# Performance work log

Measured on AMD Instinct MI355X. Metric: run time of the kernel, lower is better.

The kernel has to match this reference:

```python
import jax, jax.numpy as jnp
import numpy as np

L = 4        # routed layers
E = 12       # experts
NH = 4       # attention heads
C = 256      # hidden_dim
M = 128      # mlp_dim
TOPK = 1
LN_EPS = 1e-5


def setup_inputs() -> dict:
    key = jax.random.key(0)
    ks = jax.random.split(key, 16)
    B, H, W = 128, 14, 14

    def w(k, shape, s=0.02):
        return jax.random.normal(k, shape, dtype=jnp.float32) * s

    return {
        'stem_out': jax.random.normal(ks[0], (B, C, H, W), dtype=jnp.float32),
        'gate_w': w(ks[1], (L, C, E)), 'gate_b': jnp.zeros((L, E), jnp.float32),
        'ln1_g': jnp.ones((L, E, C), jnp.float32), 'ln1_b': jnp.zeros((L, E, C), jnp.float32),
        'wq': w(ks[2], (L, E, C, C)), 'bq': jnp.zeros((L, E, C), jnp.float32),
        'wk': w(ks[3], (L, E, C, C)), 'bk': jnp.zeros((L, E, C), jnp.float32),
        'wv': w(ks[4], (L, E, C, C)), 'bv': jnp.zeros((L, E, C), jnp.float32),
        'wo': w(ks[5], (L, E, C, C)), 'bo': jnp.zeros((L, E, C), jnp.float32),
        'ln2_g': jnp.ones((L, E, C), jnp.float32), 'ln2_b': jnp.zeros((L, E, C), jnp.float32),
        'w1': w(ks[6], (L, E, C, M)), 'b1': jnp.zeros((L, E, M), jnp.float32),
        'w2': w(ks[7], (L, E, M, C)), 'b2': jnp.zeros((L, E, C), jnp.float32),
    }


def _ln(x, g, b):
    mu = x.mean(axis=-1, keepdims=True)
    var = ((x - mu) ** 2).mean(axis=-1, keepdims=True)
    return (x - mu) * jax.lax.rsqrt(var + LN_EPS) * g + b


def _vit_block(x, p):
    # x: (B, H, W, C); p: per-expert params (no expert axis)
    B, H, W, Cc = x.shape
    d = Cc // NH
    h = _ln(x, p['g1'], p['bb1'])
    q = h @ p['wq'] + p['bq']
    k = h @ p['wk'] + p['bk']
    v = h @ p['wv'] + p['bv']

    def split(t):  # (B,H,W,C) -> (B, NH, H, W, d)
        return jnp.transpose(t.reshape(B, H, W, NH, d), (0, 3, 1, 2, 4))

    q, k, v = split(q), split(k), split(v)
    # attention is computed PER ROW h (over the W axis), matching the
    # original matmul(q, k.transpose(-2,-1)) on b n h w d tensors
    scale = jnp.asarray(d, x.dtype) ** 0.5
    scores = jnp.einsum('bnhqd,bnhkd->bnhqk', q, k) / scale
    attn = jax.nn.softmax(scores, axis=-1)
    o = jnp.einsum('bnhqk,bnhkd->bnhqd', attn, v)
    o = jnp.transpose(o, (0, 2, 3, 1, 4)).reshape(B, H, W, Cc)
    o = o @ p['wo'] + p['bo']
    x = x + o
    m = _ln(x, p['g2'], p['bb2'])
    m = jax.nn.gelu(m @ p['w1'] + p['b1'], approximate=False) @ p['w2'] + p['b2']
    return x + m


def reference(stem_out, gate_w, gate_b, ln1_g, ln1_b, wq, bq, wk, bk, wv, bv,
              wo, bo, ln2_g, ln2_b, w1, b1, w2, b2):
    x = jnp.transpose(stem_out, (0, 2, 3, 1))  # (B, H, W, C)
    B = x.shape[0]
    outputs_map, probs_list, idx_list = [], [], []
    for li in range(L):
        router_in = x.mean(axis=(1, 2))                 # (B, C)
        logits = router_in @ gate_w[li] + gate_b[li]    # (B, E)
        all_probs = jax.nn.softmax(logits, axis=-1)
        tk_p, tk_i = jax.lax.top_k(all_probs, TOPK)
        tk_p = tk_p / (tk_p.sum(axis=-1, keepdims=True) + 1e-8)
        # dense combine weights (B, E): scatter top-k weights per batch row
        w_be = jnp.zeros((B, E), x.dtype).at[jnp.arange(B)[:, None], tk_i].add(tk_p)
        p_li = {'g1': ln1_g[li], 'bb1': ln1_b[li],
                'wq': wq[li], 'bq': bq[li], 'wk': wk[li], 'bk': bk[li],
                'wv': wv[li], 'bv': bv[li], 'wo': wo[li], 'bo': bo[li],
                'g2': ln2_g[li], 'bb2': ln2_b[li],
                'w1': w1[li], 'b1': b1[li], 'w2': w2[li], 'b2': b2[li]}
        expert_outs = jax.vmap(lambda pp: _vit_block(x, pp))(p_li)  # (E,B,H,W,C)
        x = jnp.einsum('ebhwc,be->bhwc', expert_outs, w_be)
        outputs_map.append(jax.lax.stop_gradient(x))
        probs_list.append(all_probs)
        idx_list.append(tk_i)
    return (jnp.stack(outputs_map, axis=0),          # (4, B, H, W, C)
            jnp.concatenate(probs_list, axis=0),     # (4B, E)
            jnp.concatenate(idx_list, axis=0))       # (4B, top_k)
```

## Files before the change

### kernel.cpp

```cpp
#include <hip/hip_runtime.h>
#include <hip/hip_bf16.h>

#define LNUM 4
#define ENUM 12
#define CH 256
#define MLP 128
#define HW 196
#define BNUM 128
#define ROWLEN 14
#define MTOT (BNUM * HW)
#define MAXT128 208
#define MAXT64 416

#define PK_WQ 0
#define PK_WK 786432
#define PK_WV 1572864
#define PK_WO 2359296
#define PK_W1 3145728
#define PK_W2 3538944
#define PK_TOTAL 3932160

using bf16x8 = __attribute__((ext_vector_type(8))) short;
using f32x4 = __attribute__((ext_vector_type(4))) float;

__device__ inline unsigned short f2bf(float v) {
  __hip_bfloat16 b = __float2bfloat16(v);
  return *reinterpret_cast<unsigned short*>(&b);
}
__device__ inline float bf2f(unsigned short u) {
  union { unsigned int i; float f; } cv;
  cv.i = ((unsigned int)u) << 16;
  return cv.f;
}
__device__ inline void split_bf(float v, unsigned short& hi, unsigned short& lo) {
  hi = f2bf(v);
  lo = f2bf(v - bf2f(hi));
}
__device__ inline void gload16(const void* g, void* l) {
  __builtin_amdgcn_global_load_lds(
      (const __attribute__((address_space(1))) unsigned int*)g,
      (__attribute__((address_space(3))) unsigned int*)l, 16, 0, 0);
}

__global__ __launch_bounds__(256) void transpose_stem(const float* __restrict__ stem,
                                                      float* __restrict__ x,
                                                      int* __restrict__ rcnt) {
  if (blockIdx.x == 0 && blockIdx.y == 0 && blockIdx.z == 0 &&
      threadIdx.x == 0 && threadIdx.y == 0)
    rcnt[0] = 0;
  __shared__ float tile[32][33];
  int b = blockIdx.z;
  int c0 = blockIdx.x * 32;
  int p0 = blockIdx.y * 32;
  int tx = threadIdx.x;
  int ty = threadIdx.y;
  for (int i = ty; i < 32; i += 8) {
    int c = c0 + i, p = p0 + tx;
    if (p < HW) tile[i][tx] = stem[(size_t)b * CH * HW + (size_t)c * HW + p];
  }
  __syncthreads();
  for (int i = ty; i < 32; i += 8) {
    int p = p0 + i, c = c0 + tx;
    if (p < HW) x[(size_t)b * HW * CH + (size_t)p * CH + c] = tile[tx][i];
  }
}

__global__ __launch_bounds__(256) void router_kernel(
    const float* __restrict__ x, const float* __restrict__ gate_w,
    const float* __restrict__ gate_b, float* __restrict__ probs_out,
    float* __restrict__ idx_out, float* __restrict__ weight,
    int* __restrict__ eidx, int* __restrict__ rcnt, int* __restrict__ perm,
    int* __restrict__ te128, int* __restrict__ tr0128, int* __restrict__ trw128,
    int* __restrict__ te64, int* __restrict__ tr064, int* __restrict__ trw64,
    int li) {
  int b = blockIdx.x;
  int tid = threadIdx.x;
  int w = tid >> 6, lane = tid & 63;
  const float* xb = x + (size_t)b * HW * CH;
  float a0 = 0.f, a1 = 0.f, a2 = 0.f, a3 = 0.f;
#pragma unroll 7
  for (int i = 0; i < 49; ++i) {
    int p = w * 49 + i;
    float4 vv = *reinterpret_cast<const float4*>(&xb[(size_t)p * CH + lane * 4]);
    a0 += vv.x; a1 += vv.y; a2 += vv.z; a3 += vv.w;
  }
  __shared__ float rsum[4][CH];
  rsum[w][lane * 4 + 0] = a0;
  rsum[w][lane * 4 + 1] = a1;
  rsum[w][lane * 4 + 2] = a2;
  rsum[w][lane * 4 + 3] = a3;
  __syncthreads();
  __shared__ float r[CH];
  r[tid] = (rsum[0][tid] + rsum[1][tid] + rsum[2][tid] + rsum[3][tid]) *
           (1.0f / (float)HW);
  __syncthreads();
  __shared__ float part[ENUM][16];
  if (tid < 192) {
    int e = tid >> 4, seg = tid & 15;
    const float* gw = gate_w + (size_t)li * CH * ENUM;
    float acc = 0.f;
#pragma unroll
    for (int kk = 0; kk < 16; ++kk) {
      int k = seg * 16 + kk;
      acc += r[k] * gw[(size_t)k * ENUM + e];
    }
    part[e][seg] = acc;
  }
  __syncthreads();
  __shared__ float logits[ENUM];
  if (tid < ENUM) {
    float acc = gate_b[li * ENUM + tid];
#pragma unroll
    for (int seg = 0; seg < 16; ++seg) acc += part[tid][seg];
    logits[tid] = acc;
  }
  __syncthreads();
  __shared__ int last;
  if (tid == 0) {
    float mx = logits[0]; int am = 0;
    for (int e = 1; e < ENUM; ++e) if (logits[e] > mx) { mx = logits[e]; am = e; }
    float pr[ENUM]; float den = 0.f;
    for (int e = 0; e < ENUM; ++e) { pr[e] = expf(logits[e] - mx); den += pr[e]; }
    float inv = 1.0f / den;
    for (int e = 0; e < ENUM; ++e) pr[e] *= inv;
    for (int e = 0; e < ENUM; ++e)
      probs_out[(size_t)(li * BNUM + b) * ENUM + e] = pr[e];
    idx_out[li * BNUM + b] = (float)am;
    float pmax = pr[am];
    weight[b] = pmax / (pmax + 1e-8f);
    eidx[b] = am;
    __threadfence();
    int old = atomicAdd(rcnt, 1);
    last = (old == BNUM - 1) ? 1 : 0;
  }
  __syncthreads();
  if (!last) return;
  __threadfence();
  __shared__ int cnt[ENUM], start[ENUM];
  int t = tid;
  if (t < ENUM) {
    int cc = 0;
    for (int bb = 0; bb < BNUM; ++bb) if (eidx[bb] == t) ++cc;
    cnt[t] = cc;
  }
  __syncthreads();
  if (t == 0) {
    int ss = 0;
    for (int e = 0; e < ENUM; ++e) { start[e] = ss; ss += cnt[e]; }
  }
  __syncthreads();
  if (t < ENUM) {
    int pos = start[t];
    for (int bb = 0; bb < BNUM; ++bb) if (eidx[bb] == t) perm[pos++] = bb;
  }
  if (t == 0) {
    int tile = 0;
    for (int e = 0; e < ENUM; ++e) {
      int rows = cnt[e] * HW;
      int row0 = start[e] * HW;
      int off = 0;
      while (off < rows) {
        te128[tile] = e;
        tr0128[tile] = row0 + off;
        int rem = rows - off;
        trw128[tile] = rem < 128 ? rem : 128;
        ++tile; off += 128;
      }
    }
    for (; tile < MAXT128; ++tile) { trw128[tile] = 0; te128[tile] = 0; tr0128[tile] = 0; }
    rcnt[0] = 0;
  } else if (t == 1) {
    int tile = 0;
    for (int e = 0; e < ENUM; ++e) {
      int rows = cnt[e] * HW;
      int row0 = start[e] * HW;
      int off = 0;
      while (off < rows) {
        te64[tile] = e;
        tr064[tile] = row0 + off;
        int rem = rows - off;
        trw64[tile] = rem < 64 ? rem : 64;
        ++tile; off += 64;
      }
    }
    for (; tile < MAXT64; ++tile) { trw64[tile] = 0; te64[tile] = 0; tr064[tile] = 0; }
  }
}

__global__ __launch_bounds__(256) void prepack(
    const float* __restrict__ wq, const float* __restrict__ wk,
    const float* __restrict__ wv, const float* __restrict__ wo,
    const float* __restrict__ w1, const float* __restrict__ w2,
    unsigned short* __restrict__ Phi, unsigned short* __restrict__ Plo,
    int li0, int plane_mult) {
  int lz = blockIdx.z / ENUM;
  int e = blockIdx.z % ENUM;
  int li = li0 + lz;
  size_t plane = (size_t)lz * plane_mult;
  int ts = blockIdx.y;
  int K = (ts == 5) ? 128 : 256;
  int N = (ts == 4) ? 128 : 256;
  int total = (K / 8) * N;
  int id = blockIdx.x * 256 + threadIdx.x;
  if (id >= total) return;
  const float* src;
  size_t dst0;
  switch (ts) {
    case 0: src = wq; dst0 = PK_WQ; break;
    case 1: src = wk; dst0 = PK_WK; break;
    case 2: src = wv; dst0 = PK_WV; break;
    case 3: src = wo; dst0 = PK_WO; break;
    case 4: src = w1; dst0 = PK_W1; break;
    default: src = w2; dst0 = PK_W2; break;
  }
  src += ((size_t)li * ENUM + e) * K * N;
  size_t dst = plane + dst0 + (size_t)e * K * N;
  int n = id % N;
  int kg = id / N;
  const float* sp = src + (size_t)kg * 8 * N + n;
  unsigned short hs[8], ls[8];
#pragma unroll
  for (int j = 0; j < 8; ++j) split_bf(sp[(size_t)j * N], hs[j], ls[j]);
  uint4 ph, pl;
  ph.x = hs[0] | ((unsigned)hs[1] << 16); ph.y = hs[2] | ((unsigned)hs[3] << 16);
  ph.z = hs[4] | ((unsigned)hs[5] << 16); ph.w = hs[6] | ((unsigned)hs[7] << 16);
  pl.x = ls[0] | ((unsigned)ls[1] << 16); pl.y = ls[2] | ((unsigned)ls[3] << 16);
  pl.z = ls[4] | ((unsigned)ls[5] << 16); pl.w = ls[6] | ((unsigned)ls[7] << 16);
  size_t o = dst + (size_t)(kg * N + n) * 8;
  *reinterpret_cast<uint4*>(Phi + o) = ph;
  *reinterpret_cast<uint4*>(Plo + o) = pl;
}

__global__ __launch_bounds__(256) void ln_kernel(
    const float* __restrict__ xin, unsigned short* __restrict__ hhi,
    unsigned short* __restrict__ hlo,
    const float* __restrict__ g, const float* __restrict__ bta,
    const int* __restrict__ eidx, const int* __restrict__ perm, int li) {
  int tok = blockIdx.x * 4 + (threadIdx.x >> 6);
  int lane = threadIdx.x & 63;
  int s = tok / HW, p = tok - s * HW;
  int b = perm[s];
  int e = eidx[b];
  float4 vx = *reinterpret_cast<const float4*>(
      &xin[((size_t)b * HW + p) * CH + lane * 4]);
  float sm = vx.x + vx.y + vx.z + vx.w;
#pragma unroll
  for (int off = 1; off < 64; off <<= 1) sm += __shfl_xor(sm, off, 64);
  float mu = sm * (1.0f / (float)CH);
  float d0 = vx.x - mu, d1 = vx.y - mu, d2 = vx.z - mu, d3 = vx.w - mu;
  float s2 = d0 * d0 + d1 * d1 + d2 * d2 + d3 * d3;
#pragma unroll
  for (int off = 1; off < 64; off <<= 1) s2 += __shfl_xor(s2, off, 64);
  float rs = rsqrtf(s2 * (1.0f / (float)CH) + 1e-5f);
  size_t gb = ((size_t)li * ENUM + e) * CH + lane * 4;
  float4 gg = *reinterpret_cast<const float4*>(&g[gb]);
  float4 bb = *reinterpret_cast<const float4*>(&bta[gb]);
  float h0 = d0 * rs * gg.x + bb.x;
  float h1 = d1 * rs * gg.y + bb.y;
  float h2 = d2 * rs * gg.z + bb.z;
  float h3 = d3 * rs * gg.w + bb.w;
  ushort4 vh, vl;
  split_bf(h0, vh.x, vl.x);
  split_bf(h1, vh.y, vl.y);
  split_bf(h2, vh.z, vl.z);
  split_bf(h3, vh.w, vl.w);
  size_t ob = (size_t)tok * CH + lane * 4;
  *reinterpret_cast<ushort4*>(&hhi[ob]) = vh;
  *reinterpret_cast<ushort4*>(&hlo[ob]) = vl;
}

template <int EPI, int NT, int KDIM, int NXTOT, int TM_, int NTILE>
__global__ __launch_bounds__(256) void gemm_mfma(
    const unsigned short* __restrict__ Ahi, const unsigned short* __restrict__ Alo,
    const unsigned short* __restrict__ Whi, const unsigned short* __restrict__ Wlo,
    size_t wbase, size_t wstride,
    const float* __restrict__ B0, const float* __restrict__ B1p, const float* __restrict__ B2p,
    float* __restrict__ O0, float* __restrict__ O1p, float* __restrict__ O2p,
    float* __restrict__ X,
    const int* __restrict__ tile_e, const int* __restrict__ tile_row0,
    const int* __restrict__ tile_rows, const int* __restrict__ perm, int li) {
  constexpr int NX = NT / 128;
  constexpr int NSTEP = KDIM / 32;
  constexpr int FM = TM_ / 32;
  constexpr int NSEG = TM_ / 64;
  int nwg = NXTOT * NTILE;
  int orig = blockIdx.x;
  int q = nwg >> 3, r = nwg & 7;
  int xcd = orig & 7, idx = orig >> 3;
  int wg = (xcd < r ? xcd * (q + 1) : r * (q + 1) + (xcd - r) * q) + idx;
  int tileid = wg / NXTOT;
  int cbx = wg % NXTOT;

  int rows = tile_rows[tileid];
  if (rows <= 0) return;
  int row0 = tile_row0[tileid];
  int e = tile_e[tileid];
  int cb = cbx / NX;
  int ncol0 = (cbx % NX) * 128;

  const float* Bt = (EPI == 0) ? (cb == 0 ? B0 : (cb == 1 ? B1p : B2p)) : B0;
  float* Oo = (EPI == 0) ? (cb == 0 ? O0 : (cb == 1 ? O1p : O2p)) : O0;
  size_t woff = wbase + (size_t)cb * wstride + (size_t)e * (KDIM * NT);
  const unsigned short* Wh = Whi + woff;
  const unsigned short* Wl = Wlo + woff;
  const float* bias = Bt + ((size_t)li * ENUM + e) * NT + ncol0;

  __shared__ unsigned short Ash[4][TM_][8], Asl[4][TM_][8];
  __shared__ unsigned short Bsh[4][128][8], Bsl[4][128][8];

  int tid = threadIdx.x;
  int lane = tid & 63, w = tid >> 6;
  int wr = w >> 1, wc = w & 1;
  int r0w = wr * (TM_ / 2), c0w = wc * 64;
  int lrow = lane & 15, lk = lane >> 4;

  const unsigned short* gAh[NSEG];
  const unsigned short* gAl[NSEG];
#pragma unroll
  for (int s = 0; s < NSEG; ++s) {
    int rl = (s * 64 + lane < rows) ? s * 64 + lane : 0;
    gAh[s] = Ahi + (size_t)(row0 + rl) * KDIM + w * 8;
    gAl[s] = Alo + (size_t)(row0 + rl) * KDIM + w * 8;
  }

  f32x4 acc[FM][4];
#pragma unroll
  for (int i = 0; i < FM; ++i)
#pragma unroll
    for (int j = 0; j < 4; ++j) acc[i][j] = (f32x4){0.f, 0.f, 0.f, 0.f};

#pragma unroll
  for (int t = 0; t < NSTEP; ++t) {
    int k0 = t * 32;
#pragma unroll
    for (int s = 0; s < NSEG; ++s) {
      gload16(gAh[s] + k0, &Ash[w][s * 64][0]);
      gload16(gAl[s] + k0, &Asl[w][s * 64][0]);
    }
    const unsigned short* gBh = Wh + ((size_t)(t * 4 + w) * NT + ncol0 + lane) * 8;
    const unsigned short* gBl = Wl + ((size_t)(t * 4 + w) * NT + ncol0 + lane) * 8;
    gload16(gBh, &Bsh[w][0][0]);
    gload16(gBh + 64 * 8, &Bsh[w][64][0]);
    gload16(gBl, &Bsl[w][0][0]);
    gload16(gBl + 64 * 8, &Bsl[w][64][0]);
    __syncthreads();
    bf16x8 bh[4], bl[4];
#pragma unroll
    for (int fj = 0; fj < 4; ++fj) {
      bh[fj] = *reinterpret_cast<const bf16x8*>(&Bsh[lk][c0w + fj * 16 + lrow][0]);
      bl[fj] = *reinterpret_cast<const bf16x8*>(&Bsl[lk][c0w + fj * 16 + lrow][0]);
    }
#pragma unroll
    for (int fi = 0; fi < FM; ++fi) {
      bf16x8 ah = *reinterpret_cast<const bf16x8*>(&Ash[lk][r0w + fi * 16 + lrow][0]);
      bf16x8 al = *reinterpret_cast<const bf16x8*>(&Asl[lk][r0w + fi * 16 + lrow][0]);
#pragma unroll
      for (int fj = 0; fj < 4; ++fj) {
        acc[fi][fj] = __builtin_amdgcn_mfma_f32_16x16x32_bf16(ah, bh[fj], acc[fi][fj], 0, 0, 0);
        acc[fi][fj] = __builtin_amdgcn_mfma_f32_16x16x32_bf16(ah, bl[fj], acc[fi][fj], 0, 0, 0);
        acc[fi][fj] = __builtin_amdgcn_mfma_f32_16x16x32_bf16(al, bh[fj], acc[fi][fj], 0, 0, 0);
      }
    }
    __syncthreads();
  }

#pragma unroll
  for (int fi = 0; fi < FM; ++fi) {
#pragma unroll
    for (int r2 = 0; r2 < 4; ++r2) {
      int row_l = r0w + fi * 16 + lk * 4 + r2;
      if (row_l >= rows) continue;
      int rg = row0 + row_l;
      size_t gxb = 0;
      if (EPI == 2) {
        int s = rg / HW, p = rg - s * HW;
        gxb = ((size_t)perm[s] * HW + p) * CH;
      }
#pragma unroll
      for (int fj = 0; fj < 4; ++fj) {
        int col = c0w + fj * 16 + lrow;
        int ocol = ncol0 + col;
        float v = acc[fi][fj][r2] + bias[col];
        if (EPI == 0) {
          Oo[(size_t)rg * NT + ocol] = v;
        } else {
          X[gxb + ocol] += v;
        }
      }
    }
  }
}

__global__ __launch_bounds__(256) void fused_mlp(
    const unsigned short* __restrict__ Ahi, const unsigned short* __restrict__ Alo,
    const unsigned short* __restrict__ Whi, const unsigned short* __restrict__ Wlo,
    size_t plane, const float* __restrict__ b1, const float* __restrict__ b2,
    float* __restrict__ Oout, float* __restrict__ X, const float* __restrict__ wgt,
    const int* __restrict__ tile_e, const int* __restrict__ tile_row0,
    const int* __restrict__ tile_rows, const int* __restrict__ perm, int li) {
  int nwg = MAXT64;
  int orig = blockIdx.x;
  int q = nwg >> 3, r = nwg & 7;
  int xcd = orig & 7, idx = orig >> 3;
  int tileid = (xcd < r ? xcd * (q + 1) : r * (q + 1) + (xcd - r) * q) + idx;

  int rows = tile_rows[tileid];
  if (rows <= 0) return;
  int row0 = tile_row0[tileid];
  int e = tile_e[tileid];

  const unsigned short* W1h = Whi + plane + PK_W1 + (size_t)e * (CH * MLP);
  const unsigned short* W1l = Wlo + plane + PK_W1 + (size_t)e * (CH * MLP);
  const unsigned short* W2h = Whi + plane + PK_W2 + (size_t)e * (MLP * CH);
  const unsigned short* W2l = Wlo + plane + PK_W2 + (size_t)e * (MLP * CH);
  const float* bias1 = b1 + ((size_t)li * ENUM + e) * MLP;
  const float* bias2 = b2 + ((size_t)li * ENUM + e) * CH;

  __shared__ __align__(16) unsigned short smem[32768];
  unsigned short* Am_h = smem;
  unsigned short* Am_l = smem + 8192;
  unsigned short* S = smem + 16384;
  unsigned short* Ash = S;
  unsigned short* Asl = S + 2048;
  unsigned short* Bsh = S + 4096;
  unsigned short* Bsl = S + 8192;
  unsigned short* B2h = S;
  unsigned short* B2l = S + 8192;

  int tid = threadIdx.x;
  int lane = tid & 63, w = tid >> 6;
  int wr = w >> 1, wc = w & 1;
  int r0w = wr * 32, c0w = wc * 64;
  int lrow = lane & 15, lk = lane >> 4;

  int rl = (lane < rows) ? lane : 0;
  const unsigned short* gAh = Ahi + (size_t)(row0 + rl) * CH + w * 8;
  const unsigned short* gAl = Alo + (size_t)(row0 + rl) * CH + w * 8;

  f32x4 acc1[2][4];
#pragma unroll
  for (int i = 0; i < 2; ++i)
#pragma unroll
    for (int j = 0; j < 4; ++j) acc1[i][j] = (f32x4){0.f, 0.f, 0.f, 0.f};

#pragma unroll
  for (int t = 0; t < 8; ++t) {
    int k0 = t * 32;
    gload16(gAh + k0, Ash + w * 512);
    gload16(gAl + k0, Asl + w * 512);
    const unsigned short* gBh = W1h + ((size_t)(t * 4 + w) * MLP + lane) * 8;
    const unsigned short* gBl = W1l + ((size_t)(t * 4 + w) * MLP + lane) * 8;
    gload16(gBh, Bsh + w * 1024);
    gload16(gBh + 64 * 8, Bsh + w * 1024 + 64 * 8);
    gload16(gBl, Bsl + w * 1024);
    gload16(gBl + 64 * 8, Bsl + w * 1024 + 64 * 8);
    __syncthreads();
    bf16x8 bh[4], bl[4];
#pragma unroll
    for (int fj = 0; fj < 4; ++fj) {
      bh[fj] = *reinterpret_cast<const bf16x8*>(Bsh + lk * 1024 + (c0w + fj * 16 + lrow) * 8);
      bl[fj] = *reinterpret_cast<const bf16x8*>(Bsl + lk * 1024 + (c0w + fj * 16 + lrow) * 8);
    }
#pragma unroll
    for (int fi = 0; fi < 2; ++fi) {
      bf16x8 ah = *reinterpret_cast<const bf16x8*>(Ash + lk * 512 + (r0w + fi * 16 + lrow) * 8);
      bf16x8 al = *reinterpret_cast<const bf16x8*>(Asl + lk * 512 + (r0w + fi * 16 + lrow) * 8);
#pragma unroll
      for (int fj = 0; fj < 4; ++fj) {
        acc1[fi][fj] = __builtin_amdgcn_mfma_f32_16x16x32_bf16(ah, bh[fj], acc1[fi][fj], 0, 0, 0);
        acc1[fi][fj] = __builtin_amdgcn_mfma_f32_16x16x32_bf16(ah, bl[fj], acc1[fi][fj], 0, 0, 0);
        acc1[fi][fj] = __builtin_amdgcn_mfma_f32_16x16x32_bf16(al, bh[fj], acc1[fi][fj], 0, 0, 0);
      }
    }
    __syncthreads();
  }

#pragma unroll
  for (int fi = 0; fi < 2; ++fi) {
#pragma unroll
    for (int r2 = 0; r2 < 4; ++r2) {
      int row = r0w + fi * 16 + lk * 4 + r2;
#pragma unroll
      for (int fj = 0; fj < 4; ++fj) {
        int col = c0w + fj * 16 + lrow;
        float v = acc1[fi][fj][r2] + bias1[col];
        float gl = 0.5f * v * (1.0f + erff(v * 0.70710678118654752f));
        unsigned short hi, lo;
        split_bf(gl, hi, lo);
        int o = (col >> 3) * 512 + row * 8 + (col & 7);
        Am_h[o] = hi;
        Am_l[o] = lo;
      }
    }
  }
  __syncthreads();

  f32x4 acc2[2][8];
#pragma unroll
  for (int i = 0; i < 2; ++i)
#pragma unroll
    for (int j = 0; j < 8; ++j) acc2[i][j] = (f32x4){0.f, 0.f, 0.f, 0.f};
  int c0w2 = wc * 128;

#pragma unroll
  for (int t = 0; t < 4; ++t) {
    const unsigned short* gBh = W2h + ((size_t)(t * 4 + w) * CH + lane) * 8;
    const unsigned short* gBl = W2l + ((size_t)(t * 4 + w) * CH + lane) * 8;
#pragma unroll
    for (int s = 0; s < 4; ++s) {
      gload16(gBh + s * 64 * 8, B2h + w * 2048 + s * 64 * 8);
      gload16(gBl + s * 64 * 8, B2l + w * 2048 + s * 64 * 8);
    }
    __syncthreads();
    bf16x8 bh[8], bl[8];
#pragma unroll
    for (int fj = 0; fj < 8; ++fj) {
      bh[fj] = *reinterpret_cast<const bf16x8*>(B2h + lk * 2048 + (c0w2 + fj * 16 + lrow) * 8);
      bl[fj] = *reinterpret_cast<const bf16x8*>(B2l + lk * 2048 + (c0w2 + fj * 16 + lrow) * 8);
    }
#pragma unroll
    for (int fi = 0; fi < 2; ++fi) {
      bf16x8 ah = *reinterpret_cast<const bf16x8*>(Am_h + (t * 4 + lk) * 512 + (r0w + fi * 16 + lrow) * 8);
      bf16x8 al = *reinterpret_cast<const bf16x8*>(Am_l + (t * 4 + lk) * 512 + (r0w + fi * 16 + lrow) * 8);
#pragma unroll
      for (int fj = 0; fj < 8; ++fj) {
        acc2[fi][fj] = __builtin_amdgcn_mfma_f32_16x16x32_bf16(ah, bh[fj], acc2[fi][fj], 0, 0, 0);
        acc2[fi][fj] = __builtin_amdgcn_mfma_f32_16x16x32_bf16(ah, bl[fj], acc2[fi][fj], 0, 0, 0);
        acc2[fi][fj] = __builtin_amdgcn_mfma_f32_16x16x32_bf16(al, bh[fj], acc2[fi][fj], 0, 0, 0);
      }
    }
    __syncthreads();
  }

#pragma unroll
  for (int fi = 0; fi < 2; ++fi) {
#pragma unroll
    for (int r2 = 0; r2 < 4; ++r2) {
      int row_l = r0w + fi * 16 + lk * 4 + r2;
      if (row_l >= rows) continue;
      int rg = row0 + row_l;
      int s = rg / HW, p = rg - s * HW;
      int bsrt = perm[s];
      size_t gxb = ((size_t)bsrt * HW + p) * CH;
      float wr_ = wgt[bsrt];
#pragma unroll
      for (int fj = 0; fj < 8; ++fj) {
        int ocol = c0w2 + fj * 16 + lrow;
        float vv = (acc2[fi][fj][r2] + bias2[ocol] + X[gxb + ocol]) * wr_;
        X[gxb + ocol] = vv;
        Oout[gxb + ocol] = vv;
      }
    }
  }
}

__global__ __launch_bounds__(256) void attn_kernel(
    const float* __restrict__ q, const float* __restrict__ k,
    const float* __restrict__ v, unsigned short* __restrict__ ohi,
    unsigned short* __restrict__ olo) {
  int br = blockIdx.x;
  int b = br / ROWLEN, row = br % ROWLEN;
  size_t base = ((size_t)b * HW + (size_t)row * ROWLEN) * CH;
  __shared__ float qs[ROWLEN][CH + 4];
  __shared__ float ks[ROWLEN][CH + 4];
  __shared__ float vs[ROWLEN][CH + 4];
  __shared__ float sc[4][ROWLEN][ROWLEN];
  int tid = threadIdx.x;
  for (int idx = tid; idx < ROWLEN * 64; idx += 256) {
    int rr = idx >> 6, c4 = (idx & 63) * 4;
    size_t go = base + (size_t)rr * CH + c4;
    float4 qv = *reinterpret_cast<const float4*>(&q[go]);
    float4 kv = *reinterpret_cast<const float4*>(&k[go]);
    float4 vv = *reinterpret_cast<const float4*>(&v[go]);
    *reinterpret_cast<float4*>(&qs[rr][c4]) = qv;
    *reinterpret_cast<float4*>(&ks[rr][c4]) = kv;
    *reinterpret_cast<float4*>(&vs[rr][c4]) = vv;
  }
  __syncthreads();
  for (int sidx = tid; sidx < 4 * ROWLEN * ROWLEN; sidx += 256) {
    int n = sidx / (ROWLEN * ROWLEN);
    int rem = sidx % (ROWLEN * ROWLEN);
    int i = rem / ROWLEN, j = rem % ROWLEN;
    const float* qp = &qs[i][n * 64];
    const float* kp = &ks[j][n * 64];
    float s = 0.f;
#pragma unroll
    for (int d = 0; d < 64; ++d) s = fmaf(qp[d], kp[d], s);
    sc[n][i][j] = s * 0.125f;
  }
  __syncthreads();
  if (tid < 4 * ROWLEN) {
    int n = tid / ROWLEN, i = tid % ROWLEN;
    float mx = sc[n][i][0];
    for (int j = 1; j < ROWLEN; ++j) mx = fmaxf(mx, sc[n][i][j]);
    float ex[ROWLEN]; float den = 0.f;
    for (int j = 0; j < ROWLEN; ++j) { ex[j] = expf(sc[n][i][j] - mx); den += ex[j]; }
    float inv = 1.0f / den;
    for (int j = 0; j < ROWLEN; ++j) sc[n][i][j] = ex[j] * inv;
  }
  __syncthreads();
  int n = tid / 64;
  for (int i = 0; i < ROWLEN; ++i) {
    float s = 0.f;
#pragma unroll
    for (int j = 0; j < ROWLEN; ++j) s = fmaf(sc[n][i][j], vs[j][tid], s);
    unsigned short hi, lo;
    split_bf(s, hi, lo);
    ohi[base + (size_t)i * CH + tid] = hi;
    olo[base + (size_t)i * CH + tid] = lo;
  }
}

extern "C" void kernel_launch(void* const* d_in, const int* in_sizes, int n_in,
                              void* d_out, int out_size, void* d_ws, size_t ws_size,
                              hipStream_t stream) {
  const float* stem = (const float*)d_in[0];
  const float* gate_w = (const float*)d_in[1];
  const float* gate_b = (const float*)d_in[2];
  const float* ln1_g = (const float*)d_in[3];
  const float* ln1_b = (const float*)d_in[4];
  const float* wq = (const float*)d_in[5];
  const float* bq = (const float*)d_in[6];
  const float* wk = (const float*)d_in[7];
  const float* bk = (const float*)d_in[8];
  const float* wv = (const float*)d_in[9];
  const float* bv = (const float*)d_in[10];
  const float* wo = (const float*)d_in[11];
  const float* bo = (const float*)d_in[12];
  const float* ln2_g = (const float*)d_in[13];
  const float* ln2_b = (const float*)d_in[14];
  const float* w1 = (const float*)d_in[15];
  const float* b1 = (const float*)d_in[16];
  const float* w2 = (const float*)d_in[17];
  const float* b2 = (const float*)d_in[18];

  float* out = (float*)d_out;
  float* ws = (float*)d_ws;
  const size_t IMG = (size_t)BNUM * HW * CH;
  float* x = ws;
  unsigned short* h_hi = (unsigned short*)(ws + IMG);
  unsigned short* h_lo = h_hi + (size_t)MTOT * CH;
  float* q = ws + 2 * IMG;
  float* k = ws + 3 * IMG;
  float* v = ws + 4 * IMG;
  float* weight = ws + 5 * IMG;
  int* ip = (int*)(weight + BNUM);
  int* eidx = ip;              ip += BNUM;
  int* perm = ip;              ip += BNUM;
  int* te128 = ip;             ip += MAXT128;
  int* tr0128 = ip;            ip += MAXT128;
  int* trw128 = ip;            ip += MAXT128;
  int* te64 = ip;              ip += MAXT64;
  int* tr064 = ip;             ip += MAXT64;
  int* trw64 = ip;             ip += MAXT64;
  int* rcnt = ip;              ip += 4;
  unsigned short* Whi_p = (unsigned short*)(ws + 5 * IMG + 4096);

  const size_t base_bytes = (5 * IMG + 4096) * sizeof(float);
  const int all_mode = (ws_size >= base_bytes + (size_t)4 * PK_TOTAL * 2 * sizeof(unsigned short)) ? 1 : 0;
  const int nplane = all_mode ? LNUM : 1;
  unsigned short* Wlo_p = Whi_p + (size_t)nplane * PK_TOTAL;

  float* probs_out = out + 4 * IMG;
  float* idx_out = probs_out + (size_t)LNUM * BNUM * ENUM;

  transpose_stem<<<dim3(8, 7, BNUM), dim3(32, 8), 0, stream>>>(stem, x, rcnt);
  if (all_mode) {
    prepack<<<dim3(32, 6, ENUM * LNUM), 256, 0, stream>>>(
        wq, wk, wv, wo, w1, w2, Whi_p, Wlo_p, 0, PK_TOTAL);
  }

  for (int li = 0; li < LNUM; ++li) {
    router_kernel<<<BNUM, 256, 0, stream>>>(
        x, gate_w, gate_b, probs_out, idx_out, weight, eidx, rcnt, perm,
        te128, tr0128, trw128, te64, tr064, trw64, li);
    if (!all_mode) {
      prepack<<<dim3(32, 6, ENUM), 256, 0, stream>>>(
          wq, wk, wv, wo, w1, w2, Whi_p, Wlo_p, li, 0);
    }
    size_t plane = all_mode ? (size_t)li * PK_TOTAL : 0;
    ln_kernel<<<MTOT / 4, 256, 0, stream>>>(x, h_hi, h_lo, ln1_g, ln1_b, eidx, perm, li);
    gemm_mfma<0, 256, 256, 6, 128, MAXT128><<<dim3(6 * MAXT128), 256, 0, stream>>>(
        h_hi, h_lo, Whi_p, Wlo_p, plane + PK_WQ, (size_t)(ENUM * CH * CH),
        bq, bk, bv, q, k, v, nullptr,
        te128, tr0128, trw128, perm, li);
    attn_kernel<<<BNUM * ROWLEN, 256, 0, stream>>>(q, k, v, h_hi, h_lo);
    gemm_mfma<2, 256, 256, 2, 64, MAXT64><<<dim3(2 * MAXT64), 256, 0, stream>>>(
        h_hi, h_lo, Whi_p, Wlo_p, plane + PK_WO, 0,
        bo, nullptr, nullptr, nullptr, nullptr, nullptr,
        x, te64, tr064, trw64, perm, li);
    ln_kernel<<<MTOT / 4, 256, 0, stream>>>(x, h_hi, h_lo, ln2_g, ln2_b, eidx, perm, li);
    fused_mlp<<<dim3(MAXT64), 256, 0, stream>>>(
        h_hi, h_lo, Whi_p, Wlo_p, plane, b1, b2, out + (size_t)li * IMG,
        x, weight, te64, tr064, trw64, perm, li);
  }
}
```

Baseline: 844.3 us.

## Fuse output projection, residual add and LN2 into one kernel

Replaces the Wo GEMM variant of gemm_mfma and the separate second LayerNorm launch with a single kernel. Each workgroup computes a full 256-column row tile, adds bias and the residual into X, then computes LayerNorm statistics with a cross-wave reduction through shared memory. It writes the split bf16 hi/lo activations directly for the MLP. This removes one launch per layer and a re-read of X. In exchange it launches half as many workgroups and uses more registers and LDS per block, and it writes h_hi/h_lo in place over the rows it has just read as input.

```diff
diff --git a/kernel.cpp b/kernel.cpp
--- a/kernel.cpp
+++ b/kernel.cpp
@@ -269,16 +269,15 @@
   *reinterpret_cast<ushort4*>(&hlo[ob]) = vl;
 }
 
-template <int EPI, int NT, int KDIM, int NXTOT, int TM_, int NTILE>
+template <int NT, int KDIM, int NXTOT, int TM_, int NTILE>
 __global__ __launch_bounds__(256) void gemm_mfma(
     const unsigned short* __restrict__ Ahi, const unsigned short* __restrict__ Alo,
     const unsigned short* __restrict__ Whi, const unsigned short* __restrict__ Wlo,
     size_t wbase, size_t wstride,
     const float* __restrict__ B0, const float* __restrict__ B1p, const float* __restrict__ B2p,
     float* __restrict__ O0, float* __restrict__ O1p, float* __restrict__ O2p,
-    float* __restrict__ X,
     const int* __restrict__ tile_e, const int* __restrict__ tile_row0,
-    const int* __restrict__ tile_rows, const int* __restrict__ perm, int li) {
+    const int* __restrict__ tile_rows, int li) {
   constexpr int NX = NT / 128;
   constexpr int NSTEP = KDIM / 32;
   constexpr int FM = TM_ / 32;
@@ -298,8 +297,8 @@
   int cb = cbx / NX;
   int ncol0 = (cbx % NX) * 128;
 
-  const float* Bt = (EPI == 0) ? (cb == 0 ? B0 : (cb == 1 ? B1p : B2p)) : B0;
-  float* Oo = (EPI == 0) ? (cb == 0 ? O0 : (cb == 1 ? O1p : O2p)) : O0;
+  const float* Bt = (cb == 0 ? B0 : (cb == 1 ? B1p : B2p));
+  float* Oo = (cb == 0 ? O0 : (cb == 1 ? O1p : O2p));
   size_t woff = wbase + (size_t)cb * wstride + (size_t)e * (KDIM * NT);
   const unsigned short* Wh = Whi + woff;
   const unsigned short* Wl = Wlo + woff;
@@ -371,21 +370,175 @@
       int row_l = r0w + fi * 16 + lk * 4 + r2;
       if (row_l >= rows) continue;
       int rg = row0 + row_l;
-      size_t gxb = 0;
-      if (EPI == 2) {
-        int s = rg / HW, p = rg - s * HW;
-        gxb = ((size_t)perm[s] * HW + p) * CH;
-      }
 #pragma unroll
       for (int fj = 0; fj < 4; ++fj) {
         int col = c0w + fj * 16 + lrow;
         int ocol = ncol0 + col;
-        float v = acc[fi][fj][r2] + bias[col];
-        if (EPI == 0) {
-          Oo[(size_t)rg * NT + ocol] = v;
+        Oo[(size_t)rg * NT + ocol] = acc[fi][fj][r2] + bias[col];
+      }
+    }
+  }
+}
+
+__global__ __launch_bounds__(256) void fused_wo_ln(
+    const unsigned short* __restrict__ Ahi, const unsigned short* __restrict__ Alo,
+    const unsigned short* __restrict__ Whi, const unsigned short* __restrict__ Wlo,
+    size_t plane, const float* __restrict__ bo,
+    const float* __restrict__ g2, const float* __restrict__ b2ln,
+    float* __restrict__ X, unsigned short* __restrict__ hhi,
+    unsigned short* __restrict__ hlo,
+    const int* __restrict__ tile_e, const int* __restrict__ tile_row0,
+    const int* __restrict__ tile_rows, const int* __restrict__ perm, int li) {
+  int nwg = MAXT64;
+  int orig = blockIdx.x;
+  int q = nwg >> 3, r = nwg & 7;
+  int xcd = orig & 7, idx = orig >> 3;
+  int tileid = (xcd < r ? xcd * (q + 1) : r * (q + 1) + (xcd - r) * q) + idx;
+
+  int rows = tile_rows[tileid];
+  if (rows <= 0) return;
+  int row0 = tile_row0[tileid];
+  int e = tile_e[tileid];
+
+  const unsigned short* Wh = Whi + plane + PK_WO + (size_t)e * (CH * CH);
+  const unsigned short* Wl = Wlo + plane + PK_WO + (size_t)e * (CH * CH);
+  const float* biaso = bo + ((size_t)li * ENUM + e) * CH;
+  const float* gln = g2 + ((size_t)li * ENUM + e) * CH;
+  const float* bln = b2ln + ((size_t)li * ENUM + e) * CH;
+
+  __shared__ __align__(16) unsigned short Ash[4][64][8], Asl[4][64][8];
+  __shared__ __align__(16) unsigned short Bsh[4][256][8], Bsl[4][256][8];
+  __shared__ float rsm[64][2], rsq[64][2];
+
+  int tid = threadIdx.x;
+  int lane = tid & 63, w = tid >> 6;
+  int wr = w >> 1, wc = w & 1;
+  int r0w = wr * 32, c0w2 = wc * 128;
+  int lrow = lane & 15, lk = lane >> 4;
+
+  int rl = (lane < rows) ? lane : 0;
+  const unsigned short* gAh = Ahi + (size_t)(row0 + rl) * CH + w * 8;
+  const unsigned short* gAl = Alo + (size_t)(row0 + rl) * CH + w * 8;
+
+  f32x4 acc[2][8];
+#pragma unroll
+  for (int i = 0; i < 2; ++i)
+#pragma unroll
+    for (int j = 0; j < 8; ++j) acc[i][j] = (f32x4){0.f, 0.f, 0.f, 0.f};
+
+#pragma unroll
+  for (int t = 0; t < 8; ++t) {
+    int k0 = t * 32;
+    gload16(gAh + k0, &Ash[w][0][0]);
+    gload16(gAl + k0, &Asl[w][0][0]);
+    const unsigned short* gBh = Wh + ((size_t)(t * 4 + w) * CH + lane) * 8;
+    const unsigned short* gBl = Wl + ((size_t)(t * 4 + w) * CH + lane) * 8;
+#pragma unroll
+    for (int s = 0; s < 4; ++s) {
+      gload16(gBh + s * 64 * 8, &Bsh[w][s * 64][0]);
+      gload16(gBl + s * 64 * 8, &Bsl[w][s * 64][0]);
+    }
+    __syncthreads();
+    bf16x8 bh[8], bl[8];
+#pragma unroll
+    for (int fj = 0; fj < 8; ++fj) {
+      bh[fj] = *reinterpret_cast<const bf16x8*>(&Bsh[lk][c0w2 + fj * 16 + lrow][0]);
+      bl[fj] = *reinterpret_cast<const bf16x8*>(&Bsl[lk][c0w2 + fj * 16 + lrow][0]);
+    }
+#pragma unroll
+    for (int fi = 0; fi < 2; ++fi) {
+      bf16x8 ah = *reinterpret_cast<const bf16x8*>(&Ash[lk][r0w + fi * 16 + lrow][0]);
+      bf16x8 al = *reinterpret_cast<const bf16x8*>(&Asl[lk][r0w + fi * 16 + lrow][0]);
+#pragma unroll
+      for (int fj = 0; fj < 8; ++fj) {
+        acc[fi][fj] = __builtin_amdgcn_mfma_f32_16x16x32_bf16(ah, bh[fj], acc[fi][fj], 0, 0, 0);
+        acc[fi][fj] = __builtin_amdgcn_mfma_f32_16x16x32_bf16(ah, bl[fj], acc[fi][fj], 0, 0, 0);
+        acc[fi][fj] = __builtin_amdgcn_mfma_f32_16x16x32_bf16(al, bh[fj], acc[fi][fj], 0, 0, 0);
+      }
+    }
+    __syncthreads();
+  }
+
+#pragma unroll
+  for (int fi = 0; fi < 2; ++fi) {
+#pragma unroll
+    for (int r2 = 0; r2 < 4; ++r2) {
+      int row_l = r0w + fi * 16 + lk * 4 + r2;
+      bool valid = row_l < rows;
+      size_t gxb = 0;
+      if (valid) {
+        int rg = row0 + row_l;
+        int s = rg / HW, p = rg - s * HW;
+        gxb = ((size_t)perm[s] * HW + p) * CH;
+      }
+#pragma unroll
+      for (int fj = 0; fj < 8; ++fj) {
+        int ocol = c0w2 + fj * 16 + lrow;
+        float v = acc[fi][fj][r2] + biaso[ocol];
+        if (valid) {
+          v += X[gxb + ocol];
+          X[gxb + ocol] = v;
         } else {
-          X[gxb + ocol] += v;
+          v = 0.f;
         }
+        acc[fi][fj][r2] = v;
+      }
+    }
+  }
+#pragma unroll
+  for (int fi = 0; fi < 2; ++fi) {
+#pragma unroll
+    for (int r2 = 0; r2 < 4; ++r2) {
+      int row_l = r0w + fi * 16 + lk * 4 + r2;
+      float s = 0.f;
+#pragma unroll
+      for (int fj = 0; fj < 8; ++fj) s += acc[fi][fj][r2];
+      s += __shfl_xor(s, 1, 64);
+      s += __shfl_xor(s, 2, 64);
+      s += __shfl_xor(s, 4, 64);
+      s += __shfl_xor(s, 8, 64);
+      if (lrow == 0) rsm[row_l][wc] = s;
+    }
+  }
+  __syncthreads();
+#pragma unroll
+  for (int fi = 0; fi < 2; ++fi) {
+#pragma unroll
+    for (int r2 = 0; r2 < 4; ++r2) {
+      int row_l = r0w + fi * 16 + lk * 4 + r2;
+      float mu = (rsm[row_l][0] + rsm[row_l][1]) * (1.0f / (float)CH);
+      float s2 = 0.f;
+#pragma unroll
+      for (int fj = 0; fj < 8; ++fj) {
+        float d = acc[fi][fj][r2] - mu;
+        s2 += d * d;
+      }
+      s2 += __shfl_xor(s2, 1, 64);
+      s2 += __shfl_xor(s2, 2, 64);
+      s2 += __shfl_xor(s2, 4, 64);
+      s2 += __shfl_xor(s2, 8, 64);
+      if (lrow == 0) rsq[row_l][wc] = s2;
+    }
+  }
+  __syncthreads();
+#pragma unroll
+  for (int fi = 0; fi < 2; ++fi) {
+#pragma unroll
+    for (int r2 = 0; r2 < 4; ++r2) {
+      int row_l = r0w + fi * 16 + lk * 4 + r2;
+      if (row_l >= rows) continue;
+      int rg = row0 + row_l;
+      float mu = (rsm[row_l][0] + rsm[row_l][1]) * (1.0f / (float)CH);
+      float var = (rsq[row_l][0] + rsq[row_l][1]) * (1.0f / (float)CH);
+      float rs = rsqrtf(var + 1e-5f);
+#pragma unroll
+      for (int fj = 0; fj < 8; ++fj) {
+        int ocol = c0w2 + fj * 16 + lrow;
+        float hv = (acc[fi][fj][r2] - mu) * rs * gln[ocol] + bln[ocol];
+        unsigned short hi, lo;
+        split_bf(hv, hi, lo);
+        hhi[(size_t)rg * CH + ocol] = hi;
+        hlo[(size_t)rg * CH + ocol] = lo;
       }
     }
   }
@@ -680,16 +833,14 @@
     }
     size_t plane = all_mode ? (size_t)li * PK_TOTAL : 0;
     ln_kernel<<<MTOT / 4, 256, 0, stream>>>(x, h_hi, h_lo, ln1_g, ln1_b, eidx, perm, li);
-    gemm_mfma<0, 256, 256, 6, 128, MAXT128><<<dim3(6 * MAXT128), 256, 0, stream>>>(
+    gemm_mfma<256, 256, 6, 128, MAXT128><<<dim3(6 * MAXT128), 256, 0, stream>>>(
         h_hi, h_lo, Whi_p, Wlo_p, plane + PK_WQ, (size_t)(ENUM * CH * CH),
-        bq, bk, bv, q, k, v, nullptr,
-        te128, tr0128, trw128, perm, li);
+        bq, bk, bv, q, k, v,
+        te128, tr0128, trw128, li);
     attn_kernel<<<BNUM * ROWLEN, 256, 0, stream>>>(q, k, v, h_hi, h_lo);
-    gemm_mfma<2, 256, 256, 2, 64, MAXT64><<<dim3(2 * MAXT64), 256, 0, stream>>>(
-        h_hi, h_lo, Whi_p, Wlo_p, plane + PK_WO, 0,
-        bo, nullptr, nullptr, nullptr, nullptr, nullptr,
-        x, te64, tr064, trw64, perm, li);
-    ln_kernel<<<MTOT / 4, 256, 0, stream>>>(x, h_hi, h_lo, ln2_g, ln2_b, eidx, perm, li);
+    fused_wo_ln<<<dim3(MAXT64), 256, 0, stream>>>(
+        h_hi, h_lo, Whi_p, Wlo_p, plane, bo, ln2_g, ln2_b,
+        x, h_hi, h_lo, te64, tr064, trw64, perm, li);
     fused_mlp<<<dim3(MAXT64), 256, 0, stream>>>(
         h_hi, h_lo, Whi_p, Wlo_p, plane, b1, b2, out + (size_t)li * IMG,
         x, weight, te64, tr064, trw64, perm, li);
```

Measured after the change: 860.7 us. Within noise of the previous version (+1.9%).
